# Kernel tuning notes

Hardware: AMD Instinct MI355X
Metric: run time of the kernel (lower is better)

Reference implementation:

```python
import jax, jax.numpy as jnp
import numpy as np

B, L, E, H = 2, 2048, 1024, 16
D = E // H  # head_dim = 64


def setup_inputs() -> dict:
    key = jax.random.key(0)
    ks = jax.random.split(key, 9)
    s = 1.0 / np.sqrt(E)
    return {
        "query": jax.random.normal(ks[0], (B, L, E), jnp.float32),
        "key": jax.random.normal(ks[1], (B, L, E), jnp.float32),
        "value": jax.random.normal(ks[2], (B, L, E), jnp.float32),
        # torch Linear weights are [out_features, in_features]
        "Wq": jax.random.uniform(ks[3], (E, E), jnp.float32, -s, s),
        "bq": jnp.zeros((E,), jnp.float32),
        "Wk": jax.random.uniform(ks[4], (E, E), jnp.float32, -s, s),  # k_proj, no bias (add_bias_kv=False)
        "Wv": jax.random.uniform(ks[5], (E, E), jnp.float32, -s, s),  # v_proj, no bias
        "Wo": jax.random.uniform(ks[6], (E, E), jnp.float32, -s, s),
        "bo": jnp.zeros((E,), jnp.float32),
    }


def reference(query, key, value, Wq, bq, Wk, Wv, Wo, bo):
    # Projections (torch Linear: y = x @ W.T + b)
    q = query @ Wq.T + bq          # [B, L, E]
    k = key @ Wk.T                 # [B, L, E]
    v = value @ Wv.T               # [B, L, E]
    # Split heads
    q = q.reshape(B, L, H, D)
    k = k.reshape(B, L, H, D)
    v = v.reshape(B, L, H, D)
    # Scaled dot-product attention; the source's chunked online-softmax
    # computes exactly softmax(q k^T / sqrt(D)) v.
    q = q / jnp.sqrt(jnp.asarray(D, q.dtype))
    scores = jnp.einsum("bqhd,bkhd->bhqk", q, k)      # [B, H, L, L]
    probs = jax.nn.softmax(scores, axis=-1)
    out = jnp.einsum("bhqk,bkhd->bqhd", probs, v)     # [B, L, H, D]
    out = out.reshape(B, L, E)
    return out @ Wo.T + bo
```

## Files before the change

### kernel.cpp

```cpp
#include <hip/hip_runtime.h>

typedef __bf16 bf16;
typedef __bf16 bf16x8 __attribute__((ext_vector_type(8)));
typedef __bf16 bf16x4 __attribute__((ext_vector_type(4)));
typedef float  f32x4  __attribute__((ext_vector_type(4)));

#define MFMA_BF16(a, b, c) __builtin_amdgcn_mfma_f32_16x16x32_bf16((a), (b), (c), 0, 0, 0)


__device__ __forceinline__ void async_load16(const bf16* g, const bf16* l) {
    auto gp = (const __attribute__((address_space(1))) unsigned int*)(unsigned long long)(const void*)g;
    auto lp = (__attribute__((address_space(3))) unsigned int*)(unsigned int)(unsigned long long)(const void*)l;
    __builtin_amdgcn_global_load_lds(gp, lp, 16, 0, 0);
}

__global__ void cvt_bf16_kernel(
    const float* __restrict__ s0, const float* __restrict__ s1, const float* __restrict__ s2,
    const float* __restrict__ s3, const float* __restrict__ s4, const float* __restrict__ s5,
    const float* __restrict__ s6,
    bf16* __restrict__ d0, bf16* __restrict__ d1, bf16* __restrict__ d2,
    bf16* __restrict__ d3, bf16* __restrict__ d4, bf16* __restrict__ d5,
    bf16* __restrict__ d6)
{
    unsigned e = (blockIdx.x * 256 + threadIdx.x) * 4;
    const float* src; bf16* dst; unsigned off;
    if (e < 12582912u) {
        unsigned which = e >> 22;
        src = which == 0 ? s0 : (which == 1 ? s1 : s2);
        dst = which == 0 ? d0 : (which == 1 ? d1 : d2);
        off = e & 4194303u;
    } else {
        unsigned ew = e - 12582912u;
        unsigned which = ew >> 20;
        src = which == 0 ? s3 : (which == 1 ? s4 : (which == 2 ? s5 : s6));
        dst = which == 0 ? d3 : (which == 1 ? d4 : (which == 2 ? d5 : d6));
        off = ew & 1048575u;
    }
    float4 f = *(const float4*)(src + off);
    bf16x4 o;
    o.x = (bf16)f.x; o.y = (bf16)f.y; o.z = (bf16)f.z; o.w = (bf16)f.w;
    *(bf16x4*)(dst + off) = o;
}

template<int BN>
__global__ __launch_bounds__(256, (BN == 128) ? 2 : 4) void gemm4_kernel(
    const bf16* __restrict__ Xq, const bf16* __restrict__ Xk, const bf16* __restrict__ Xv,
    const bf16* __restrict__ Ao,
    const bf16* __restrict__ Wq, const bf16* __restrict__ Wk, const bf16* __restrict__ Wv,
    const bf16* __restrict__ Wo,
    const float* __restrict__ bq, const float* __restrict__ bo,
    bf16* __restrict__ Qs, bf16* __restrict__ Ksw, bf16* __restrict__ Vsw,
    float* __restrict__ out, int zbase)
{
    const int z = zbase + blockIdx.z;
    const bf16 *Amat, *Bmat;
    if (z == 0)      { Amat = Wq; Bmat = Xq; }
    else if (z == 1) { Amat = Wk; Bmat = Xk; }
    else if (z == 2) { Amat = Xv; Bmat = Wv; }
    else             { Amat = Wo; Bmat = Ao; }

    const int flat = blockIdx.x + 8 * blockIdx.y;
    const int c    = flat & 7;
    const int j    = flat >> 3;
    const int ft   = j & 7;
    const int tt   = c * (gridDim.y >> 3) + (j >> 3);

    const int m0 = (z == 2 ? tt : ft) * 128;
    const int n0 = (z == 2 ? ft : tt) * BN;

    __shared__ __align__(16) bf16 lA[2][128 * 32];
    __shared__ __align__(16) bf16 lB[2][BN * 32];

    const int tid  = threadIdx.x;
    const int w    = tid >> 6;
    const int lane = tid & 63;
    const int lm   = lane & 15;
    const int g    = lane >> 4;
    const int wm   = (w & 1) * 64;
    const int wn   = (w >> 1) * (BN / 2);
    constexpr int NT = BN / 32;
    constexpr int T  = (128 + BN) / 64;

    f32x4 acc[4][NT] = {};

    for (int kb2 = 0; kb2 < 16; kb2++) {
        __syncthreads();
#pragma unroll
        for (int st = 0; st < 2; st++) {
            int kb = kb2 * 2 + st;
#pragma unroll
            for (int t = 0; t < T; t++) {
                int s   = (t * 4 + w) * 64 + lane;
                int row = s >> 2;
                int gs  = s & 3;
                int gg  = gs ^ ((row >> 1) & 3);
                if (row < 128)
                    async_load16(Amat + (size_t)(m0 + row) * 1024 + kb * 32 + gg * 8,
                                 lA[st] + s * 8);
                else
                    async_load16(Bmat + (size_t)(n0 + row - 128) * 1024 + kb * 32 + gg * 8,
                                 lB[st] + (s - 512) * 8);
            }
        }
        __syncthreads();

#pragma unroll
        for (int st = 0; st < 2; st++) {
            bf16x8 af[4], bfr[NT];
#pragma unroll
            for (int mt = 0; mt < 4; mt++) {
                int row = wm + mt * 16 + lm;
                af[mt] = *(const bf16x8*)(lA[st] + row * 32 + ((g ^ ((row >> 1) & 3)) << 3));
            }
#pragma unroll
            for (int nt = 0; nt < NT; nt++) {
                int row = wn + nt * 16 + lm;
                bfr[nt] = *(const bf16x8*)(lB[st] + row * 32 + ((g ^ ((row >> 1) & 3)) << 3));
            }
#pragma unroll
            for (int mt = 0; mt < 4; mt++)
#pragma unroll
                for (int nt = 0; nt < NT; nt++)
                    acc[mt][nt] = MFMA_BF16(af[mt], bfr[nt], acc[mt][nt]);
        }
    }

    if (z == 3) {
#pragma unroll
        for (int mt = 0; mt < 4; mt++) {
            int mb = m0 + wm + mt * 16 + g * 4;
            f32x4 bov = *(const f32x4*)(bo + mb);
#pragma unroll
            for (int nt = 0; nt < NT; nt++) {
                int n = n0 + wn + nt * 16 + lm;
                f32x4 val;
#pragma unroll
                for (int r = 0; r < 4; r++) val[r] = acc[mt][nt][r] + bov[r];
                *(f32x4*)(out + (size_t)n * 1024 + mb) = val;
            }
        }
    } else if (z == 2) {
#pragma unroll
        for (int mt = 0; mt < 4; mt++) {
            int mb   = m0 + wm + mt * 16 + g * 4;
            int b    = mb >> 11;
            int lpos = mb & 2047;
            int kb2  = lpos >> 6, kc = (lpos >> 5) & 1, gv = (lpos >> 3) & 3, j0 = lpos & 7;
#pragma unroll
            for (int nt = 0; nt < NT; nt++) {
                int n = n0 + wn + nt * 16 + lm;
                int h = n >> 6, mt2 = (n >> 4) & 3, lmv = n & 15;
                bf16x4 ov;
#pragma unroll
                for (int r = 0; r < 4; r++) ov[r] = (bf16)acc[mt][nt][r];
                *(bf16x4*)(Vsw + (size_t)(b * 16 + h) * 131072 +
                           (size_t)((kb2 * 8 + mt2 * 2 + kc) * 64 + gv * 16 + lmv) * 8 + j0) = ov;
            }
        }
    } else if (z == 1) {
#pragma unroll
        for (int mt = 0; mt < 4; mt++) {
            int mb = m0 + wm + mt * 16 + g * 4;
            int h  = mb >> 6;
            int f  = (mb >> 5) & 1, gk = (mb >> 3) & 3, j0 = mb & 7;
#pragma unroll
            for (int nt = 0; nt < NT; nt++) {
                int n    = n0 + wn + nt * 16 + lm;
                int b    = n >> 11;
                int lpos = n & 2047;
                int kb2  = lpos >> 6;
                int rem  = lpos & 63;
                int cc   = ((rem >> 4) & 2) | ((rem >> 2) & 1);
                int lmk  = ((rem >> 1) & 12) | (rem & 3);
                bf16x4 ov;
#pragma unroll
                for (int r = 0; r < 4; r++) ov[r] = (bf16)acc[mt][nt][r];
                *(bf16x4*)(Ksw + (size_t)(b * 16 + h) * 131072 +
                           (size_t)((kb2 * 8 + cc * 2 + f) * 64 + gk * 16 + lmk) * 8 + j0) = ov;
            }
        }
    } else {
        const float qscale = 0.18033688011112042f;
#pragma unroll
        for (int mt = 0; mt < 4; mt++) {
            int mb  = m0 + wm + mt * 16 + g * 4;
            int h   = mb >> 6;
            int dd0 = mb & 63;
            f32x4 bqv = *(const f32x4*)(bq + mb);
#pragma unroll
            for (int nt = 0; nt < NT; nt++) {
                int n    = n0 + wn + nt * 16 + lm;
                int b    = n >> 11;
                int lpos = n & 2047;
                bf16x4 ov;
#pragma unroll
                for (int r = 0; r < 4; r++)
                    ov[r] = (bf16)((acc[mt][nt][r] + bqv[r]) * qscale);
                *(bf16x4*)(Qs + (size_t)((b * 16 + h) * 2048 + lpos) * 64 + dd0) = ov;
            }
        }
    }
}

__global__ __launch_bounds__(256, 2) void attn_kernel(
    const bf16* __restrict__ Qs, const bf16* __restrict__ Ksw,
    const bf16* __restrict__ Vsw, bf16* __restrict__ attn)
{
    const int tid  = threadIdx.x;
    const int w    = tid >> 6;
    const int lane = tid & 63;
    const int lm   = lane & 15;
    const int g    = lane >> 4;
    const int i    = blockIdx.x;
    const int bh   = ((i & 7) << 2) | ((i >> 3) & 3);
    const int q0   = (i >> 5) * 128 + w * 32;

    const bf16* Qh = Qs  + (size_t)bh * 131072;
    const bf16* Kh = Ksw + (size_t)bh * 131072;
    const bf16* Vh = Vsw + (size_t)bh * 131072;

    __shared__ __align__(16) bf16 ost[4][32 * 72];

    bf16x8 qf[2][2];
#pragma unroll
    for (int qi = 0; qi < 2; qi++)
#pragma unroll
        for (int f = 0; f < 2; f++)
            qf[qi][f] = *(const bf16x8*)(Qh + (size_t)(q0 + qi * 16 + lm) * 64 + f * 32 + g * 8);

    const f32x4 fzero = {0.0f, 0.0f, 0.0f, 0.0f};
    f32x4 o[2][4] = {};
    float lsum[2] = {0.0f, 0.0f};

    bf16x8 kf[8], vf[8];
#pragma unroll
    for (int t = 0; t < 8; t++)
        kf[t] = *(const bf16x8*)(Kh + ((size_t)t * 64 + lane) * 8);
#pragma unroll
    for (int t = 0; t < 8; t++)
        vf[t] = *(const bf16x8*)(Vh + ((size_t)t * 64 + lane) * 8);

    for (int kb = 0; kb < 32; kb++) {
        const int kn = (kb < 31) ? kb + 1 : 31;
        const bf16* Kn = Kh + (size_t)kn * 4096;
        const bf16* Vn = Vh + (size_t)kn * 4096;

        f32x4 s[2][4];
        __builtin_amdgcn_s_setprio(1);
#pragma unroll
        for (int c = 0; c < 4; c++) {
            s[0][c] = MFMA_BF16(kf[2 * c],     qf[0][0], fzero);
            s[1][c] = MFMA_BF16(kf[2 * c],     qf[1][0], fzero);
            s[0][c] = MFMA_BF16(kf[2 * c + 1], qf[0][1], s[0][c]);
            s[1][c] = MFMA_BF16(kf[2 * c + 1], qf[1][1], s[1][c]);
        }
        __builtin_amdgcn_s_setprio(0);

#pragma unroll
        for (int t = 0; t < 8; t++)
            kf[t] = *(const bf16x8*)(Kn + ((size_t)t * 64 + lane) * 8);

        bf16x8 pb[2][2];
#pragma unroll
        for (int qi = 0; qi < 2; qi++) {
            float part = 0.0f;
#pragma unroll
            for (int kc = 0; kc < 2; kc++)
#pragma unroll
                for (int r = 0; r < 4; r++) {
                    float p0 = __builtin_amdgcn_exp2f(s[qi][2 * kc][r]);
                    float p1 = __builtin_amdgcn_exp2f(s[qi][2 * kc + 1][r]);
                    pb[qi][kc][r]     = (bf16)p0;
                    pb[qi][kc][r + 4] = (bf16)p1;
                    part += p0 + p1;
                }
            lsum[qi] += part;
        }

        __builtin_amdgcn_s_setprio(1);
#pragma unroll
        for (int kc = 0; kc < 2; kc++)
#pragma unroll
            for (int mt = 0; mt < 4; mt++) {
                o[0][mt] = MFMA_BF16(vf[mt * 2 + kc], pb[0][kc], o[0][mt]);
                o[1][mt] = MFMA_BF16(vf[mt * 2 + kc], pb[1][kc], o[1][mt]);
            }
        __builtin_amdgcn_s_setprio(0);

#pragma unroll
        for (int t = 0; t < 8; t++)
            vf[t] = *(const bf16x8*)(Vn + ((size_t)t * 64 + lane) * 8);
    }

#pragma unroll
    for (int qi = 0; qi < 2; qi++) {
        lsum[qi] += __shfl_xor(lsum[qi], 16);
        lsum[qi] += __shfl_xor(lsum[qi], 32);
    }

    const int b = bh >> 4, h = bh & 15;
#pragma unroll
    for (int qi = 0; qi < 2; qi++) {
        float inv = 1.0f / lsum[qi];
#pragma unroll
        for (int mt = 0; mt < 4; mt++) {
            bf16x4 ov;
#pragma unroll
            for (int r = 0; r < 4; r++) ov[r] = (bf16)(o[qi][mt][r] * inv);
            *(bf16x4*)(ost[w] + (qi * 16 + lm) * 72 + mt * 16 + g * 4) = ov;
        }
    }
#pragma unroll
    for (int it = 0; it < 4; it++) {
        int cc = it * 64 + lane;
        int q  = cc >> 3, ch = cc & 7;
        bf16x8 t = *(const bf16x8*)(ost[w] + q * 72 + ch * 8);
        *(bf16x8*)(attn + (size_t)(b * 2048 + q0 + q) * 1024 + h * 64 + ch * 8) = t;
    }
}

extern "C" void kernel_launch(void* const* d_in, const int* in_sizes, int n_in,
                              void* d_out, int out_size, void* d_ws, size_t ws_size,
                              hipStream_t stream) {
    const float* query = (const float*)d_in[0];
    const float* key   = (const float*)d_in[1];
    const float* value = (const float*)d_in[2];
    const float* Wq    = (const float*)d_in[3];
    const float* bq    = (const float*)d_in[4];
    const float* Wk    = (const float*)d_in[5];
    const float* Wv    = (const float*)d_in[6];
    const float* Wo    = (const float*)d_in[7];
    const float* bo    = (const float*)d_in[8];

    char* ws = (char*)d_ws;
    bf16* Xq  = (bf16*)(ws);
    bf16* Xk  = (bf16*)(ws + ((size_t)8  << 20));
    bf16* Xv  = (bf16*)(ws + ((size_t)16 << 20));
    bf16* Wqb = (bf16*)(ws + ((size_t)24 << 20));
    bf16* Wkb = (bf16*)(ws + ((size_t)26 << 20));
    bf16* Wvb = (bf16*)(ws + ((size_t)28 << 20));
    bf16* Wob = (bf16*)(ws + ((size_t)30 << 20));
    bf16* Qs  = (bf16*)(ws + ((size_t)32 << 20));
    bf16* Ksw = (bf16*)(ws + ((size_t)40 << 20));
    bf16* Vsw = (bf16*)(ws + ((size_t)48 << 20));
    bf16* attn = Xq;

    cvt_bf16_kernel<<<dim3(16384, 1, 1), 256, 0, stream>>>(
        query, key, value, Wq, Wk, Wv, Wo, Xq, Xk, Xv, Wqb, Wkb, Wvb, Wob);

    gemm4_kernel<128><<<dim3(8, 32, 3), 256, 0, stream>>>(
        Xq, Xk, Xv, attn, Wqb, Wkb, Wvb, Wob, bq, bo, Qs, Ksw, Vsw, (float*)d_out, 0);

    attn_kernel<<<dim3(512, 1, 1), 256, 0, stream>>>(Qs, Ksw, Vsw, attn);

    gemm4_kernel<64><<<dim3(8, 64, 1), 256, 0, stream>>>(
        Xq, Xk, Xv, attn, Wqb, Wkb, Wvb, Wob, bq, bo, Qs, Ksw, Vsw, (float*)d_out, 3);
}
```

Measured before the change: 206.3 us.

## Stage K/V tiles through triple-buffered LDS with async global-to-LDS loads

Replaces the per-wave register prefetch of K and V tiles from global memory with a cooperative triple-buffered LDS pipeline. Each wave issues a quarter of the tile loads through global_load_lds, and the loop uses waitcnt plus a barrier before reading fragments from LDS. Before the change, all four waves loaded the same K/V tiles separately, so this cuts redundant global/L2 traffic and register pressure. The cost is 48KB more LDS per block, which may limit occupancy, plus a block-wide barrier every iteration and extra LDS reads.

```diff
diff --git a/kernel.cpp b/kernel.cpp
--- a/kernel.cpp
+++ b/kernel.cpp
@@ -219,6 +219,8 @@
     const bf16* Kh = Ksw + (size_t)bh * 131072;
     const bf16* Vh = Vsw + (size_t)bh * 131072;
 
+    __shared__ __align__(16) bf16 kbuf[3][4096];
+    __shared__ __align__(16) bf16 vbuf[3][4096];
     __shared__ __align__(16) bf16 ost[4][32 * 72];
 
     bf16x8 qf[2][2];
@@ -227,38 +229,57 @@
 #pragma unroll
         for (int f = 0; f < 2; f++)
             qf[qi][f] = *(const bf16x8*)(Qh + (size_t)(q0 + qi * 16 + lm) * 64 + f * 32 + g * 8);
+
+#define STAGE(sb, buf)                                                          \
+    do {                                                                        \
+        _Pragma("unroll")                                                       \
+        for (int t = 0; t < 4; t++) {                                           \
+            int slot = w * 4 + t;                                               \
+            if (slot < 8)                                                       \
+                async_load16(Kh + ((size_t)((sb) * 8 + slot) * 64 + lane) * 8,  \
+                             kbuf[buf] + (slot * 64 + lane) * 8);               \
+            else                                                                \
+                async_load16(Vh + ((size_t)((sb) * 8 + slot - 8) * 64 + lane) * 8, \
+                             vbuf[buf] + ((slot - 8) * 64 + lane) * 8);         \
+        }                                                                       \
+    } while (0)
+
+    STAGE(0, 0);
+    STAGE(1, 1);
 
     const f32x4 fzero = {0.0f, 0.0f, 0.0f, 0.0f};
     f32x4 o[2][4] = {};
     float lsum[2] = {0.0f, 0.0f};
 
-    bf16x8 kf[8], vf[8];
-#pragma unroll
-    for (int t = 0; t < 8; t++)
-        kf[t] = *(const bf16x8*)(Kh + ((size_t)t * 64 + lane) * 8);
-#pragma unroll
-    for (int t = 0; t < 8; t++)
-        vf[t] = *(const bf16x8*)(Vh + ((size_t)t * 64 + lane) * 8);
-
+    int cur = 0;
     for (int kb = 0; kb < 32; kb++) {
-        const int kn = (kb < 31) ? kb + 1 : 31;
-        const bf16* Kn = Kh + (size_t)kn * 4096;
-        const bf16* Vn = Vh + (size_t)kn * 4096;
+        if (kb < 31)
+            asm volatile("s_waitcnt vmcnt(4)" ::: "memory");
+        else
+            asm volatile("s_waitcnt vmcnt(0)" ::: "memory");
+        __builtin_amdgcn_s_barrier();
+        __builtin_amdgcn_sched_barrier(0);
+
+        if (kb < 30) {
+            int nb = cur + 2; if (nb >= 3) nb -= 3;
+            STAGE(kb + 2, nb);
+        }
+
+        const bf16* kc_ = kbuf[cur];
+        const bf16* vc_ = vbuf[cur];
 
         f32x4 s[2][4];
         __builtin_amdgcn_s_setprio(1);
 #pragma unroll
         for (int c = 0; c < 4; c++) {
-            s[0][c] = MFMA_BF16(kf[2 * c],     qf[0][0], fzero);
-            s[1][c] = MFMA_BF16(kf[2 * c],     qf[1][0], fzero);
-            s[0][c] = MFMA_BF16(kf[2 * c + 1], qf[0][1], s[0][c]);
-            s[1][c] = MFMA_BF16(kf[2 * c + 1], qf[1][1], s[1][c]);
+            bf16x8 kf0 = *(const bf16x8*)(kc_ + ((c * 2 + 0) * 64 + lane) * 8);
+            bf16x8 kf1 = *(const bf16x8*)(kc_ + ((c * 2 + 1) * 64 + lane) * 8);
+            s[0][c] = MFMA_BF16(kf0, qf[0][0], fzero);
+            s[1][c] = MFMA_BF16(kf0, qf[1][0], fzero);
+            s[0][c] = MFMA_BF16(kf1, qf[0][1], s[0][c]);
+            s[1][c] = MFMA_BF16(kf1, qf[1][1], s[1][c]);
         }
         __builtin_amdgcn_s_setprio(0);
-
-#pragma unroll
-        for (int t = 0; t < 8; t++)
-            kf[t] = *(const bf16x8*)(Kn + ((size_t)t * 64 + lane) * 8);
 
         bf16x8 pb[2][2];
 #pragma unroll
@@ -282,15 +303,15 @@
         for (int kc = 0; kc < 2; kc++)
 #pragma unroll
             for (int mt = 0; mt < 4; mt++) {
-                o[0][mt] = MFMA_BF16(vf[mt * 2 + kc], pb[0][kc], o[0][mt]);
-                o[1][mt] = MFMA_BF16(vf[mt * 2 + kc], pb[1][kc], o[1][mt]);
+                bf16x8 vf = *(const bf16x8*)(vc_ + ((mt * 2 + kc) * 64 + lane) * 8);
+                o[0][mt] = MFMA_BF16(vf, pb[0][kc], o[0][mt]);
+                o[1][mt] = MFMA_BF16(vf, pb[1][kc], o[1][mt]);
             }
         __builtin_amdgcn_s_setprio(0);
 
-#pragma unroll
-        for (int t = 0; t < 8; t++)
-            vf[t] = *(const bf16x8*)(Vn + ((size_t)t * 64 + lane) * 8);
-    }
+        cur += 1; if (cur >= 3) cur -= 3;
+    }
+#undef STAGE
 
 #pragma unroll
     for (int qi = 0; qi < 2; qi++) {
```

Measured after the change: 205.1 us. About the same (-0.6%).
